# Kernel optimization log

Measured on AMD Instinct MI355X. Metric: run time of the kernel, lower is better.

Reference implementation:

```python
import jax, jax.numpy as jnp
import numpy as np

NEG_SLOPE = 0.2


def _gcn_conv(x, edge_index, W, b):
    # Standard GCNConv: y = D^-1/2 (A + I) D^-1/2 (x W) + b
    N = x.shape[0]
    loop = jnp.arange(N, dtype=edge_index.dtype)
    src = jnp.concatenate([edge_index[0], loop])  # [E+N]
    dst = jnp.concatenate([edge_index[1], loop])  # [E+N]
    deg = jax.ops.segment_sum(jnp.ones_like(dst, dtype=x.dtype), dst, num_segments=N)
    dinv = jnp.where(deg > 0, jax.lax.rsqrt(deg), 0.0)
    norm = dinv[src] * dinv[dst]                  # [E+N]
    h = x @ W                                     # [N, out] dense GEMM
    msg = h[src] * norm[:, None]                  # irregular gather, [E+N, out]
    agg = jax.ops.segment_sum(msg, dst, num_segments=N)  # irregular scatter
    return agg + b


def setup_inputs() -> dict:
    key = jax.random.key(0)
    ks = jax.random.split(key, 5)
    N, E, d_in, d_hid = 50000, 800000, 256, 512
    s = lambda fan_in, fan_out: np.sqrt(6.0 / (fan_in + fan_out))
    return {
        "x": jax.random.normal(ks[0], (N, d_in), dtype=jnp.float32),
        "edge_index": jax.random.randint(ks[1], (2, E), 0, N, dtype=jnp.int64),
        "W_gcn": jax.random.uniform(ks[2], (d_in, d_hid), jnp.float32, -s(d_in, d_hid), s(d_in, d_hid)),
        "b_gcn": jnp.zeros((d_hid,), jnp.float32),
        "W2": jax.random.uniform(ks[3], (d_hid, d_hid), jnp.float32, -s(d_hid, d_hid), s(d_hid, d_hid)),
        "b2": jnp.zeros((d_hid,), jnp.float32),
        "W_out": jax.random.uniform(ks[4], (d_hid, 1), jnp.float32, -s(d_hid, 1), s(d_hid, 1)),
        "b_out": jnp.zeros((1,), jnp.float32),
    }


def reference(x, edge_index, W_gcn, b_gcn, W2, b2, W_out, b_out):
    h = _gcn_conv(x, edge_index, W_gcn, b_gcn)           # [N, 512]
    h = jax.nn.leaky_relu(h, NEG_SLOPE)
    h = jax.nn.leaky_relu(h @ W2 + b2, NEG_SLOPE)        # [N, 512]
    return h @ W_out + b_out                             # [N, 1]
```

## Files before the change

### kernel.cpp

```cpp
#include <hip/hip_runtime.h>

#define D_IN  256
#define D_HID 512
#define NEG_SLOPE 0.2f
#define SCAN_CHUNK 2048
#define GATHER_BLOCKS 2048

typedef __attribute__((ext_vector_type(8))) short short8;
typedef __attribute__((ext_vector_type(4))) float floatx4;

__device__ __forceinline__ unsigned short f2bf(float f) {
    unsigned int u = __float_as_uint(f);
    u += 0x7fffu + ((u >> 16) & 1u);
    return (unsigned short)(u >> 16);
}
__device__ __forceinline__ float bf2f(unsigned short u) {
    return __uint_as_float(((unsigned int)u) << 16);
}

__device__ __forceinline__ int eidx(const void* ei, long pos, int is64) {
    return is64 ? (int)((const long long*)ei)[pos] : ((const int*)ei)[pos];
}

__global__ __launch_bounds__(256) void k_init(int* __restrict__ deg, int N,
                                              const unsigned int* __restrict__ ei,
                                              int npairs, int* flag,
                                              const float* __restrict__ b_out,
                                              float* __restrict__ out) {
    int t = blockIdx.x * blockDim.x + threadIdx.x;
    if (blockIdx.x == 0) {
        __shared__ int nz;
        if (threadIdx.x == 0) nz = 0;
        __syncthreads();
        for (int p = threadIdx.x; p < npairs; p += blockDim.x)
            if (ei[2 * p + 1] != 0) nz = 1;
        __syncthreads();
        if (threadIdx.x == 0) *flag = nz ? 0 : 1;
    }
    if (t < N) { deg[t] = 0; out[t] = b_out[0]; }
}

__global__ __launch_bounds__(256) void k_wtrans(const float* __restrict__ Wa,
                                                unsigned short* __restrict__ Wat,
                                                const float* __restrict__ Wb,
                                                unsigned short* __restrict__ Wbt) {
    __shared__ float t[64][65];
    int b = blockIdx.x;
    const float* W; unsigned short* Wt; int K, Nc, tk, tn;
    if (b < 32) { W = Wa; Wt = Wat; K = 256; Nc = 512; tk = b & 3; tn = b >> 2; }
    else { b -= 32; W = Wb; Wt = Wbt; K = 512; Nc = 512; tk = b & 7; tn = b >> 3; }
    int k0 = tk * 64, n0 = tn * 64;
    int c = threadIdx.x & 63;
    int r0 = threadIdx.x >> 6;
#pragma unroll
    for (int i = 0; i < 16; ++i) {
        int r = r0 + i * 4;
        t[r][c] = W[(long)(k0 + r) * Nc + n0 + c];
    }
    __syncthreads();
#pragma unroll
    for (int i = 0; i < 16; ++i) {
        int r = r0 + i * 4;
        Wt[(long)(n0 + r) * K + k0 + c] = f2bf(t[c][r]);
    }
}

__global__ void k_deg_count(const void* __restrict__ ei, const int* __restrict__ flag,
                            int* __restrict__ deg, int E) {
    int e = blockIdx.x * blockDim.x + threadIdx.x;
    if (e < E) atomicAdd(&deg[eidx(ei, (long)E + e, *flag)], 1);
}

__global__ __launch_bounds__(256) void k_scan1(const int* __restrict__ deg,
                                               int* __restrict__ bsum, int N) {
    int base = blockIdx.x * SCAN_CHUNK;
    int hi = min(base + SCAN_CHUNK, N);
    int s = 0;
    for (int i = base + threadIdx.x; i < hi; i += 256) s += deg[i];
#pragma unroll
    for (int off = 32; off > 0; off >>= 1) s += __shfl_down(s, off, 64);
    __shared__ int lds[4];
    if ((threadIdx.x & 63) == 0) lds[threadIdx.x >> 6] = s;
    __syncthreads();
    if (threadIdx.x == 0) bsum[blockIdx.x] = lds[0] + lds[1] + lds[2] + lds[3];
}

__global__ __launch_bounds__(256) void k_scan23(const int* __restrict__ deg,
                                                const int* __restrict__ bsum, int NB,
                                                int* __restrict__ offs,
                                                int* __restrict__ cursor,
                                                float* __restrict__ dinv, int N) {
    __shared__ int lds[256];
    int t = threadIdx.x;
    int bbase = 0;
    for (int i = 0; i < NB; ++i) bbase += (i < blockIdx.x) ? bsum[i] : 0;
    if (blockIdx.x == NB - 1 && t == 0) offs[N] = bbase + bsum[NB - 1];
    int base = blockIdx.x * SCAN_CHUNK;
    int lo = base + t * 8;
    int v[8], s = 0;
#pragma unroll
    for (int j = 0; j < 8; ++j) {
        int i = lo + j;
        v[j] = (i < N) ? deg[i] : 0;
        s += v[j];
    }
    lds[t] = s;
    __syncthreads();
    for (int d = 1; d < 256; d <<= 1) {
        int add = (t >= d) ? lds[t - d] : 0;
        __syncthreads();
        lds[t] += add;
        __syncthreads();
    }
    int run = bbase + ((t > 0) ? lds[t - 1] : 0);
#pragma unroll
    for (int j = 0; j < 8; ++j) {
        int i = lo + j;
        if (i < N) {
            offs[i] = run; cursor[i] = run;
            dinv[i] = rsqrtf(1.0f + (float)v[j]);
            run += v[j];
        }
    }
}

__global__ __launch_bounds__(256) void k_prescale(const float* __restrict__ x,
                                                  const float* __restrict__ dinv,
                                                  unsigned short* __restrict__ xb, int N) {
    long t = (long)blockIdx.x * blockDim.x + threadIdx.x;
    long total = (long)N * D_IN / 4;
    if (t >= total) return;
    int row = (int)(t >> 6);
    float s = dinv[row];
    float4 v = *(const float4*)(x + t * 4);
    ushort4 o;
    o.x = f2bf(v.x * s); o.y = f2bf(v.y * s); o.z = f2bf(v.z * s); o.w = f2bf(v.w * s);
    *(ushort4*)(xb + t * 4) = o;
}

__global__ void k_fill(const void* __restrict__ ei, const int* __restrict__ flag,
                       int* __restrict__ cursor, int* __restrict__ esrc, int E) {
    int e = blockIdx.x * blockDim.x + threadIdx.x;
    if (e >= E) return;
    int is64 = *flag;
    int s = eidx(ei, e, is64), d = eidx(ei, (long)E + e, is64);
    int pos = atomicAdd(&cursor[d], 1);
    esrc[pos] = s;
}

__global__ __launch_bounds__(256) void k_gather(const unsigned short* __restrict__ xb,
                                                const int* __restrict__ offs,
                                                const int* __restrict__ esrc,
                                                const float* __restrict__ dinv,
                                                unsigned short* __restrict__ aggb,
                                                int N, int nwaves) {
    int wid = blockIdx.x * 4 + (threadIdx.x >> 6);
    int lo = (int)((long)wid * N / nwaves);
    int hi = (int)((long)(wid + 1) * N / nwaves);
    if (lo >= hi) return;
    int lane = threadIdx.x & 63;
    int half = lane >> 5;
    int colofs = (lane & 31) * 8;
    const unsigned short* xbc = xb + colofs;

    int node = lo;
    int bg = offs[node];
    int en = offs[node + 1];
    float di = dinv[node];
    short8 sv = *(const short8*)(xbc + (long)node * D_IN);

    while (true) {
        int nxt = node + 1;
        bool has = nxt < hi;
        int en2 = 0; float di2 = 0.f; short8 sv2;
        if (has) {
            en2 = offs[nxt + 1];
            di2 = dinv[nxt];
            sv2 = *(const short8*)(xbc + (long)nxt * D_IN);
        }

        float a[8];
#pragma unroll
        for (int j = 0; j < 8; ++j)
            a[j] = (half == 0) ? bf2f((unsigned short)sv[j]) : 0.f;

        int e = bg;
        for (; e + 8 <= en; e += 8) {
            int s0 = esrc[e + half];
            int s1 = esrc[e + 2 + half];
            int s2 = esrc[e + 4 + half];
            int s3 = esrc[e + 6 + half];
            short8 u0 = *(const short8*)(xbc + (long)s0 * D_IN);
            short8 u1 = *(const short8*)(xbc + (long)s1 * D_IN);
            short8 u2 = *(const short8*)(xbc + (long)s2 * D_IN);
            short8 u3 = *(const short8*)(xbc + (long)s3 * D_IN);
#pragma unroll
            for (int j = 0; j < 8; ++j) {
                float t0 = bf2f((unsigned short)u0[j]) + bf2f((unsigned short)u1[j]);
                float t1 = bf2f((unsigned short)u2[j]) + bf2f((unsigned short)u3[j]);
                a[j] += t0 + t1;
            }
        }
        for (; e < en; e += 2) {
            int j0 = e + half;
            int jj = (j0 < en) ? j0 : en - 1;
            int s = esrc[jj];
            float w = (j0 < en) ? 1.f : 0.f;
            short8 u = *(const short8*)(xbc + (long)s * D_IN);
#pragma unroll
            for (int j = 0; j < 8; ++j)
                a[j] += w * bf2f((unsigned short)u[j]);
        }

#pragma unroll
        for (int j = 0; j < 8; ++j) a[j] += __shfl_xor(a[j], 32, 64);

        if (half == 0) {
            short8 o;
#pragma unroll
            for (int j = 0; j < 8; ++j) o[j] = (short)f2bf(a[j] * di);
            *(short8*)(aggb + (long)node * D_IN + colofs) = o;
        }

        if (!has) break;
        node = nxt; bg = en; en = en2; di = di2; sv = sv2;
    }
}

__device__ __forceinline__ void async_cp16(const unsigned short* gp, unsigned short* lp) {
    __builtin_amdgcn_global_load_lds((const __attribute__((address_space(1))) void*)gp,
                                     (__attribute__((address_space(3))) void*)lp, 16, 0, 0);
}

__device__ __forceinline__ void stage_sw64(const unsigned short* src, int strideK,
                                           int rowMax, unsigned short* lds, int tid) {
#pragma unroll
    for (int rr = 0; rr < 4; ++rr) {
        int c = rr * 256 + tid;
        int row = c >> 3;
        int ci = (c & 7) ^ (row & 7);
        if (row > rowMax) row = rowMax;
        async_cp16(src + (long)row * strideK + ci * 8, lds + c * 8);
    }
}

__device__ __forceinline__ bool map_block(int b, int M, int& m0, int& n0) {
    int x = b & 7, slot = b >> 3;
    int mt = x + 8 * (slot >> 2);
    m0 = mt * 128; n0 = (slot & 3) * 128;
    return m0 < M;
}

__global__ __launch_bounds__(256) void k_gemm_bf16(const unsigned short* __restrict__ A,
                                                   const unsigned short* __restrict__ Bt,
                                                   const float* __restrict__ bias,
                                                   unsigned short* __restrict__ C,
                                                   int M, int K) {
    __shared__ __align__(16) unsigned short As[128 * 64];
    __shared__ __align__(16) unsigned short Bs[128 * 64];
    __shared__ __align__(16) unsigned short Ep[32 * 128];
    const int tid  = threadIdx.x;
    const int lane = tid & 63, wave = tid >> 6;
    int m0, n0;
    if (!map_block(blockIdx.x, M, m0, n0)) return;
    const int r = lane & 15, q = lane >> 4;
    const int xv = r & 7;
    const int wm = (wave & 1) * 64, wn = (wave >> 1) * 64;
    const int band = wm >> 6;

    floatx4 acc[4][4];
#pragma unroll
    for (int i = 0; i < 4; ++i)
#pragma unroll
        for (int j = 0; j < 4; ++j) acc[i][j] = (floatx4){0.f, 0.f, 0.f, 0.f};

    for (int k0 = 0; k0 < K; k0 += 64) {
        stage_sw64(A + (long)m0 * K + k0, K, M - 1 - m0, As, tid);
        stage_sw64(Bt + (long)n0 * K + k0, K, 127, Bs, tid);
        __syncthreads();

#pragma unroll
        for (int s = 0; s < 2; ++s) {
            int slotbase = s * 4 + q;
            short8 af[4], bf[4];
#pragma unroll
            for (int i = 0; i < 4; ++i)
                af[i] = *(const short8*)(As + (wm + i * 16 + r) * 64 + (slotbase ^ xv) * 8);
#pragma unroll
            for (int j = 0; j < 4; ++j)
                bf[j] = *(const short8*)(Bs + (wn + j * 16 + r) * 64 + (slotbase ^ xv) * 8);
#pragma unroll
            for (int i = 0; i < 4; ++i)
#pragma unroll
                for (int j = 0; j < 4; ++j)
                    acc[i][j] = __builtin_amdgcn_mfma_f32_16x16x32_bf16(af[i], bf[j], acc[i][j], 0, 0, 0);
        }
        __syncthreads();
    }

    float bv[4];
#pragma unroll
    for (int j = 0; j < 4; ++j) bv[j] = bias[n0 + wn + j * 16 + r];

#pragma unroll
    for (int i = 0; i < 4; ++i) {
#pragma unroll
        for (int j = 0; j < 4; ++j) {
#pragma unroll
            for (int t2 = 0; t2 < 4; ++t2) {
                float v = acc[i][j][t2] + bv[j];
                v = v > 0.f ? v : NEG_SLOPE * v;
                Ep[(band * 16 + q * 4 + t2) * 128 + wn + j * 16 + r] = f2bf(v);
            }
        }
        __syncthreads();
#pragma unroll
        for (int rr = 0; rr < 2; ++rr) {
            int c = rr * 256 + tid;
            int lrow = c >> 4, ccol = c & 15;
            int grow = m0 + (lrow >> 4) * 64 + i * 16 + (lrow & 15);
            if (grow < M) {
                short8 v = *(const short8*)(Ep + lrow * 128 + ccol * 8);
                *(short8*)(C + (long)grow * D_HID + n0 + ccol * 8) = v;
            }
        }
        __syncthreads();
    }
}

__global__ __launch_bounds__(256) void k_gemm2f(const unsigned short* __restrict__ A,
                                                const unsigned short* __restrict__ Bt,
                                                const float* __restrict__ bias,
                                                const float* __restrict__ wout,
                                                float* __restrict__ out,
                                                int M, int K) {
    __shared__ __align__(16) unsigned short As[128 * 64];
    __shared__ __align__(16) unsigned short Bs[128 * 64];
    const int tid  = threadIdx.x;
    const int lane = tid & 63, wave = tid >> 6;
    int m0, n0;
    if (!map_block(blockIdx.x, M, m0, n0)) return;
    const int r = lane & 15, q = lane >> 4;
    const int xv = r & 7;
    const int wm = (wave & 1) * 64, wn = (wave >> 1) * 64;

    floatx4 acc[4][4];
#pragma unroll
    for (int i = 0; i < 4; ++i)
#pragma unroll
        for (int j = 0; j < 4; ++j) acc[i][j] = (floatx4){0.f, 0.f, 0.f, 0.f};

    for (int k0 = 0; k0 < K; k0 += 64) {
        stage_sw64(A + (long)m0 * K + k0, K, M - 1 - m0, As, tid);
        stage_sw64(Bt + (long)n0 * K + k0, K, 127, Bs, tid);
        __syncthreads();

#pragma unroll
        for (int s = 0; s < 2; ++s) {
            int slotbase = s * 4 + q;
            short8 af[4], bf[4];
#pragma unroll
            for (int i = 0; i < 4; ++i)
                af[i] = *(const short8*)(As + (wm + i * 16 + r) * 64 + (slotbase ^ xv) * 8);
#pragma unroll
            for (int j = 0; j < 4; ++j)
                bf[j] = *(const short8*)(Bs + (wn + j * 16 + r) * 64 + (slotbase ^ xv) * 8);
#pragma unroll
            for (int i = 0; i < 4; ++i)
#pragma unroll
                for (int j = 0; j < 4; ++j)
                    acc[i][j] = __builtin_amdgcn_mfma_f32_16x16x32_bf16(af[i], bf[j], acc[i][j], 0, 0, 0);
        }
        __syncthreads();
    }

    float bv[4], wv[4];
#pragma unroll
    for (int j = 0; j < 4; ++j) {
        int col = n0 + wn + j * 16 + r;
        bv[j] = bias[col];
        wv[j] = wout[col];
    }
#pragma unroll
    for (int i = 0; i < 4; ++i) {
#pragma unroll
        for (int t2 = 0; t2 < 4; ++t2) {
            float p = 0.f;
#pragma unroll
            for (int j = 0; j < 4; ++j) {
                float v = acc[i][j][t2] + bv[j];
                v = v > 0.f ? v : NEG_SLOPE * v;
                p += v * wv[j];
            }
            p += __shfl_xor(p, 8, 64);
            p += __shfl_xor(p, 4, 64);
            p += __shfl_xor(p, 2, 64);
            p += __shfl_xor(p, 1, 64);
            if (r == 0) {
                int row = m0 + wm + i * 16 + q * 4 + t2;
                if (row < M) atomicAdd(&out[row], p);
            }
        }
    }
}

extern "C" void kernel_launch(void* const* d_in, const int* in_sizes, int n_in,
                              void* d_out, int out_size, void* d_ws, size_t ws_size,
                              hipStream_t stream) {
    const float* x     = (const float*)d_in[0];
    const void*  ei    = d_in[1];
    const float* W_gcn = (const float*)d_in[2];
    const float* b_gcn = (const float*)d_in[3];
    const float* W2    = (const float*)d_in[4];
    const float* b2    = (const float*)d_in[5];
    const float* W_out = (const float*)d_in[6];
    const float* b_out = (const float*)d_in[7];
    float* out = (float*)d_out;

    const int N = in_sizes[0] / D_IN;
    const int E = in_sizes[1] / 2;
    const int NB = (N + SCAN_CHUNK - 1) / SCAN_CHUNK;

    char* w = (char*)d_ws;
    size_t off = 0;
    auto alloc = [&](size_t bytes) { char* p = w + off; off = (off + bytes + 255) & ~(size_t)255; return p; };
    int*            flag   = (int*)alloc(256);
    float*          dinv   = (float*)alloc((size_t)N * 4);
    int*            deg_i  = (int*)alloc((size_t)N * 4);
    int*            offs   = (int*)alloc((size_t)(N + 1) * 4);
    int*            cursor = (int*)alloc((size_t)N * 4);
    int*            bsum   = (int*)alloc((size_t)NB * 4);
    int*            esrc   = (int*)alloc((size_t)(E + 16) * 4);
    unsigned short* xb     = (unsigned short*)alloc((size_t)N * D_IN * 2);
    unsigned short* aggb   = (unsigned short*)alloc((size_t)N * D_IN * 2);
    unsigned short* h1     = (unsigned short*)alloc((size_t)N * D_HID * 2);
    unsigned short* Wgt    = (unsigned short*)alloc((size_t)D_IN * D_HID * 2);
    unsigned short* W2t    = (unsigned short*)alloc((size_t)D_HID * D_HID * 2);

    int npairs = E < 2048 ? E : 2048;
    k_init<<<(N + 255) / 256, 256, 0, stream>>>(deg_i, N, (const unsigned int*)ei,
                                                npairs, flag, b_out, out);
    k_wtrans<<<96, 256, 0, stream>>>(W_gcn, Wgt, W2, W2t);

    k_deg_count<<<(E + 255) / 256, 256, 0, stream>>>(ei, flag, deg_i, E);
    k_scan1<<<NB, 256, 0, stream>>>(deg_i, bsum, N);
    k_scan23<<<NB, 256, 0, stream>>>(deg_i, bsum, NB, offs, cursor, dinv, N);

    long pthreads = (long)N * D_IN / 4;
    k_prescale<<<(unsigned)((pthreads + 255) / 256), 256, 0, stream>>>(x, dinv, xb, N);
    k_fill<<<(E + 255) / 256, 256, 0, stream>>>(ei, flag, cursor, esrc, E);

    int gblocks_gather = GATHER_BLOCKS;
    int nwaves = gblocks_gather * 4;
    k_gather<<<gblocks_gather, 256, 0, stream>>>(xb, offs, esrc, dinv, aggb, N, nwaves);

    int mtiles = (N + 127) / 128;
    int gblocks = ((mtiles + 7) / 8) * 8 * 4;
    k_gemm_bf16<<<gblocks, 256, 0, stream>>>(aggb, Wgt, b_gcn, h1, N, D_IN);
    k_gemm2f<<<gblocks, 256, 0, stream>>>(h1, W2t, b2, W_out, out, N, D_HID);
}
```

Before: 338.3 us.

## Merge setup kernels, use one-node-per-wave gather, double-buffer GEMM LDS tiles

Folds the weight-transpose kernel into the init kernel and the prescale and CSR-fill kernels into one launch, cutting launch count and the serialization between them. The gather kernel drops its persistent wave loop with next-node prefetch and instead launches one wave per node. Both bf16 GEMMs move to double-buffered LDS staging so the next K tile's loads are issued while MFMAs run on the current tile. This doubles LDS use per block, which may lower occupancy, and the double-buffered loop appears to drop a barrier between compute and the next stage, which risks a race on the buffer being overwritten.

```diff
diff --git a/kernel.cpp b/kernel.cpp
--- a/kernel.cpp
+++ b/kernel.cpp
@@ -4,7 +4,6 @@
 #define D_HID 512
 #define NEG_SLOPE 0.2f
 #define SCAN_CHUNK 2048
-#define GATHER_BLOCKS 2048
 
 typedef __attribute__((ext_vector_type(8))) short short8;
 typedef __attribute__((ext_vector_type(4))) float floatx4;
@@ -26,9 +25,34 @@
                                               const unsigned int* __restrict__ ei,
                                               int npairs, int* flag,
                                               const float* __restrict__ b_out,
-                                              float* __restrict__ out) {
-    int t = blockIdx.x * blockDim.x + threadIdx.x;
-    if (blockIdx.x == 0) {
+                                              float* __restrict__ out,
+                                              const float* __restrict__ Wa,
+                                              unsigned short* __restrict__ Wat,
+                                              const float* __restrict__ Wb,
+                                              unsigned short* __restrict__ Wbt) {
+    __shared__ float tl[64][65];
+    int b = blockIdx.x;
+    if (b < 96) {
+        const float* W; unsigned short* Wt; int K, Nc, tk, tn;
+        if (b < 32) { W = Wa; Wt = Wat; K = 256; Nc = 512; tk = b & 3; tn = b >> 2; }
+        else { b -= 32; W = Wb; Wt = Wbt; K = 512; Nc = 512; tk = b & 7; tn = b >> 3; }
+        int k0 = tk * 64, n0 = tn * 64;
+        int c = threadIdx.x & 63;
+        int r0 = threadIdx.x >> 6;
+#pragma unroll
+        for (int i = 0; i < 16; ++i) {
+            int r = r0 + i * 4;
+            tl[r][c] = W[(long)(k0 + r) * Nc + n0 + c];
+        }
+        __syncthreads();
+#pragma unroll
+        for (int i = 0; i < 16; ++i) {
+            int r = r0 + i * 4;
+            Wt[(long)(n0 + r) * K + k0 + c] = f2bf(tl[c][r]);
+        }
+        return;
+    }
+    if (b == 96) {
         __shared__ int nz;
         if (threadIdx.x == 0) nz = 0;
         __syncthreads();
@@ -37,32 +61,8 @@
         __syncthreads();
         if (threadIdx.x == 0) *flag = nz ? 0 : 1;
     }
+    int t = (b - 96) * 256 + threadIdx.x;
     if (t < N) { deg[t] = 0; out[t] = b_out[0]; }
-}
-
-__global__ __launch_bounds__(256) void k_wtrans(const float* __restrict__ Wa,
-                                                unsigned short* __restrict__ Wat,
-                                                const float* __restrict__ Wb,
-                                                unsigned short* __restrict__ Wbt) {
-    __shared__ float t[64][65];
-    int b = blockIdx.x;
-    const float* W; unsigned short* Wt; int K, Nc, tk, tn;
-    if (b < 32) { W = Wa; Wt = Wat; K = 256; Nc = 512; tk = b & 3; tn = b >> 2; }
-    else { b -= 32; W = Wb; Wt = Wbt; K = 512; Nc = 512; tk = b & 7; tn = b >> 3; }
-    int k0 = tk * 64, n0 = tn * 64;
-    int c = threadIdx.x & 63;
-    int r0 = threadIdx.x >> 6;
-#pragma unroll
-    for (int i = 0; i < 16; ++i) {
-        int r = r0 + i * 4;
-        t[r][c] = W[(long)(k0 + r) * Nc + n0 + c];
-    }
-    __syncthreads();
-#pragma unroll
-    for (int i = 0; i < 16; ++i) {
-        int r = r0 + i * 4;
-        Wt[(long)(n0 + r) * K + k0 + c] = f2bf(t[c][r]);
-    }
 }
 
 __global__ void k_deg_count(const void* __restrict__ ei, const int* __restrict__ flag,
@@ -124,23 +124,27 @@
     }
 }
 
-__global__ __launch_bounds__(256) void k_prescale(const float* __restrict__ x,
-                                                  const float* __restrict__ dinv,
-                                                  unsigned short* __restrict__ xb, int N) {
-    long t = (long)blockIdx.x * blockDim.x + threadIdx.x;
-    long total = (long)N * D_IN / 4;
-    if (t >= total) return;
-    int row = (int)(t >> 6);
-    float s = dinv[row];
-    float4 v = *(const float4*)(x + t * 4);
-    ushort4 o;
-    o.x = f2bf(v.x * s); o.y = f2bf(v.y * s); o.z = f2bf(v.z * s); o.w = f2bf(v.w * s);
-    *(ushort4*)(xb + t * 4) = o;
-}
-
-__global__ void k_fill(const void* __restrict__ ei, const int* __restrict__ flag,
-                       int* __restrict__ cursor, int* __restrict__ esrc, int E) {
-    int e = blockIdx.x * blockDim.x + threadIdx.x;
+__global__ __launch_bounds__(256) void k_prefill(const float* __restrict__ x,
+                                                 const float* __restrict__ dinv,
+                                                 unsigned short* __restrict__ xb,
+                                                 const void* __restrict__ ei,
+                                                 const int* __restrict__ flag,
+                                                 int* __restrict__ cursor,
+                                                 int* __restrict__ esrc,
+                                                 int N, int E, int PB) {
+    if ((int)blockIdx.x < PB) {
+        long t = (long)blockIdx.x * 256 + threadIdx.x;
+        long total = (long)N * D_IN / 4;
+        if (t >= total) return;
+        int row = (int)(t >> 6);
+        float s = dinv[row];
+        float4 v = *(const float4*)(x + t * 4);
+        ushort4 o;
+        o.x = f2bf(v.x * s); o.y = f2bf(v.y * s); o.z = f2bf(v.z * s); o.w = f2bf(v.w * s);
+        *(ushort4*)(xb + t * 4) = o;
+        return;
+    }
+    int e = (blockIdx.x - PB) * 256 + threadIdx.x;
     if (e >= E) return;
     int is64 = *flag;
     int s = eidx(ei, e, is64), d = eidx(ei, (long)E + e, is64);
@@ -152,78 +156,60 @@
                                                 const int* __restrict__ offs,
                                                 const int* __restrict__ esrc,
                                                 const float* __restrict__ dinv,
-                                                unsigned short* __restrict__ aggb,
-                                                int N, int nwaves) {
-    int wid = blockIdx.x * 4 + (threadIdx.x >> 6);
-    int lo = (int)((long)wid * N / nwaves);
-    int hi = (int)((long)(wid + 1) * N / nwaves);
-    if (lo >= hi) return;
+                                                unsigned short* __restrict__ aggb, int N) {
+    int node = blockIdx.x * 4 + (threadIdx.x >> 6);
+    if (node >= N) return;
     int lane = threadIdx.x & 63;
     int half = lane >> 5;
     int colofs = (lane & 31) * 8;
     const unsigned short* xbc = xb + colofs;
-
-    int node = lo;
-    int bg = offs[node];
-    int en = offs[node + 1];
     float di = dinv[node];
-    short8 sv = *(const short8*)(xbc + (long)node * D_IN);
-
-    while (true) {
-        int nxt = node + 1;
-        bool has = nxt < hi;
-        int en2 = 0; float di2 = 0.f; short8 sv2;
-        if (has) {
-            en2 = offs[nxt + 1];
-            di2 = dinv[nxt];
-            sv2 = *(const short8*)(xbc + (long)nxt * D_IN);
-        }
-
-        float a[8];
+
+    float a[8];
+    {
+        short8 v = *(const short8*)(xbc + (long)node * D_IN);
 #pragma unroll
         for (int j = 0; j < 8; ++j)
-            a[j] = (half == 0) ? bf2f((unsigned short)sv[j]) : 0.f;
-
-        int e = bg;
-        for (; e + 8 <= en; e += 8) {
-            int s0 = esrc[e + half];
-            int s1 = esrc[e + 2 + half];
-            int s2 = esrc[e + 4 + half];
-            int s3 = esrc[e + 6 + half];
-            short8 u0 = *(const short8*)(xbc + (long)s0 * D_IN);
-            short8 u1 = *(const short8*)(xbc + (long)s1 * D_IN);
-            short8 u2 = *(const short8*)(xbc + (long)s2 * D_IN);
-            short8 u3 = *(const short8*)(xbc + (long)s3 * D_IN);
-#pragma unroll
-            for (int j = 0; j < 8; ++j) {
-                float t0 = bf2f((unsigned short)u0[j]) + bf2f((unsigned short)u1[j]);
-                float t1 = bf2f((unsigned short)u2[j]) + bf2f((unsigned short)u3[j]);
-                a[j] += t0 + t1;
-            }
-        }
-        for (; e < en; e += 2) {
-            int j0 = e + half;
-            int jj = (j0 < en) ? j0 : en - 1;
-            int s = esrc[jj];
-            float w = (j0 < en) ? 1.f : 0.f;
-            short8 u = *(const short8*)(xbc + (long)s * D_IN);
-#pragma unroll
-            for (int j = 0; j < 8; ++j)
-                a[j] += w * bf2f((unsigned short)u[j]);
-        }
-
-#pragma unroll
-        for (int j = 0; j < 8; ++j) a[j] += __shfl_xor(a[j], 32, 64);
-
-        if (half == 0) {
-            short8 o;
-#pragma unroll
-            for (int j = 0; j < 8; ++j) o[j] = (short)f2bf(a[j] * di);
-            *(short8*)(aggb + (long)node * D_IN + colofs) = o;
-        }
-
-        if (!has) break;
-        node = nxt; bg = en; en = en2; di = di2; sv = sv2;
+            a[j] = (half == 0) ? bf2f((unsigned short)v[j]) : 0.f;
+    }
+
+    int beg = offs[node], end = offs[node + 1];
+    int e = beg;
+    for (; e + 8 <= end; e += 8) {
+        int s0 = esrc[e + half];
+        int s1 = esrc[e + 2 + half];
+        int s2 = esrc[e + 4 + half];
+        int s3 = esrc[e + 6 + half];
+        short8 u0 = *(const short8*)(xbc + (long)s0 * D_IN);
+        short8 u1 = *(const short8*)(xbc + (long)s1 * D_IN);
+        short8 u2 = *(const short8*)(xbc + (long)s2 * D_IN);
+        short8 u3 = *(const short8*)(xbc + (long)s3 * D_IN);
+#pragma unroll
+        for (int j = 0; j < 8; ++j) {
+            float t0 = bf2f((unsigned short)u0[j]) + bf2f((unsigned short)u1[j]);
+            float t1 = bf2f((unsigned short)u2[j]) + bf2f((unsigned short)u3[j]);
+            a[j] += t0 + t1;
+        }
+    }
+    for (; e < end; e += 2) {
+        int j0 = e + half;
+        int jj = (j0 < end) ? j0 : end - 1;
+        int s = esrc[jj];
+        float w = (j0 < end) ? 1.f : 0.f;
+        short8 u = *(const short8*)(xbc + (long)s * D_IN);
+#pragma unroll
+        for (int j = 0; j < 8; ++j)
+            a[j] += w * bf2f((unsigned short)u[j]);
+    }
+
+#pragma unroll
+    for (int j = 0; j < 8; ++j) a[j] += __shfl_xor(a[j], 32, 64);
+
+    if (half == 0) {
+        short8 o;
+#pragma unroll
+        for (int j = 0; j < 8; ++j) o[j] = (short)f2bf(a[j] * di);
+        *(short8*)(aggb + (long)node * D_IN + colofs) = o;
     }
 }
 
@@ -256,8 +242,8 @@
                                                    const float* __restrict__ bias,
                                                    unsigned short* __restrict__ C,
                                                    int M, int K) {
-    __shared__ __align__(16) unsigned short As[128 * 64];
-    __shared__ __align__(16) unsigned short Bs[128 * 64];
+    __shared__ __align__(16) unsigned short As[2][128 * 64];
+    __shared__ __align__(16) unsigned short Bs[2][128 * 64];
     __shared__ __align__(16) unsigned short Ep[32 * 128];
     const int tid  = threadIdx.x;
     const int lane = tid & 63, wave = tid >> 6;
@@ -267,6 +253,9 @@
     const int xv = r & 7;
     const int wm = (wave & 1) * 64, wn = (wave >> 1) * 64;
     const int band = wm >> 6;
+    const int rmA = M - 1 - m0;
+    const unsigned short* Ab = A + (long)m0 * K;
+    const unsigned short* Bb = Bt + (long)n0 * K;
 
     floatx4 acc[4][4];
 #pragma unroll
@@ -274,21 +263,26 @@
 #pragma unroll
         for (int j = 0; j < 4; ++j) acc[i][j] = (floatx4){0.f, 0.f, 0.f, 0.f};
 
-    for (int k0 = 0; k0 < K; k0 += 64) {
-        stage_sw64(A + (long)m0 * K + k0, K, M - 1 - m0, As, tid);
-        stage_sw64(Bt + (long)n0 * K + k0, K, 127, Bs, tid);
-        __syncthreads();
-
+    const int nt = K >> 6;
+    stage_sw64(Ab, K, rmA, As[0], tid);
+    stage_sw64(Bb, K, 127, Bs[0], tid);
+    __syncthreads();
+    for (int t = 0; t < nt; ++t) {
+        const int cur = t & 1;
+        if (t + 1 < nt) {
+            stage_sw64(Ab + (t + 1) * 64, K, rmA, As[cur ^ 1], tid);
+            stage_sw64(Bb + (t + 1) * 64, K, 127, Bs[cur ^ 1], tid);
+        }
 #pragma unroll
         for (int s = 0; s < 2; ++s) {
             int slotbase = s * 4 + q;
             short8 af[4], bf[4];
 #pragma unroll
             for (int i = 0; i < 4; ++i)
-                af[i] = *(const short8*)(As + (wm + i * 16 + r) * 64 + (slotbase ^ xv) * 8);
+                af[i] = *(const short8*)(As[cur] + (wm + i * 16 + r) * 64 + (slotbase ^ xv) * 8);
 #pragma unroll
             for (int j = 0; j < 4; ++j)
-                bf[j] = *(const short8*)(Bs + (wn + j * 16 + r) * 64 + (slotbase ^ xv) * 8);
+                bf[j] = *(const short8*)(Bs[cur] + (wn + j * 16 + r) * 64 + (slotbase ^ xv) * 8);
 #pragma unroll
             for (int i = 0; i < 4; ++i)
 #pragma unroll
@@ -334,8 +328,8 @@
                                                 const float* __restrict__ wout,
                                                 float* __restrict__ out,
                                                 int M, int K) {
-    __shared__ __align__(16) unsigned short As[128 * 64];
-    __shared__ __align__(16) unsigned short Bs[128 * 64];
+    __shared__ __align__(16) unsigned short As[2][128 * 64];
+    __shared__ __align__(16) unsigned short Bs[2][128 * 64];
     const int tid  = threadIdx.x;
     const int lane = tid & 63, wave = tid >> 6;
     int m0, n0;
@@ -343,6 +337,9 @@
     const int r = lane & 15, q = lane >> 4;
     const int xv = r & 7;
     const int wm = (wave & 1) * 64, wn = (wave >> 1) * 64;
+    const int rmA = M - 1 - m0;
+    const unsigned short* Ab = A + (long)m0 * K;
+    const unsigned short* Bb = Bt + (long)n0 * K;
 
     floatx4 acc[4][4];
 #pragma unroll
@@ -350,21 +347,26 @@
 #pragma unroll
         for (int j = 0; j < 4; ++j) acc[i][j] = (floatx4){0.f, 0.f, 0.f, 0.f};
 
-    for (int k0 = 0; k0 < K; k0 += 64) {
-        stage_sw64(A + (long)m0 * K + k0, K, M - 1 - m0, As, tid);
-        stage_sw64(Bt + (long)n0 * K + k0, K, 127, Bs, tid);
-        __syncthreads();
-
+    const int nt = K >> 6;
+    stage_sw64(Ab, K, rmA, As[0], tid);
+    stage_sw64(Bb, K, 127, Bs[0], tid);
+    __syncthreads();
+    for (int t = 0; t < nt; ++t) {
+        const int cur = t & 1;
+        if (t + 1 < nt) {
+            stage_sw64(Ab + (t + 1) * 64, K, rmA, As[cur ^ 1], tid);
+            stage_sw64(Bb + (t + 1) * 64, K, 127, Bs[cur ^ 1], tid);
+        }
 #pragma unroll
         for (int s = 0; s < 2; ++s) {
             int slotbase = s * 4 + q;
             short8 af[4], bf[4];
 #pragma unroll
             for (int i = 0; i < 4; ++i)
-                af[i] = *(const short8*)(As + (wm + i * 16 + r) * 64 + (slotbase ^ xv) * 8);
+                af[i] = *(const short8*)(As[cur] + (wm + i * 16 + r) * 64 + (slotbase ^ xv) * 8);
 #pragma unroll
             for (int j = 0; j < 4; ++j)
-                bf[j] = *(const short8*)(Bs + (wn + j * 16 + r) * 64 + (slotbase ^ xv) * 8);
+                bf[j] = *(const short8*)(Bs[cur] + (wn + j * 16 + r) * 64 + (slotbase ^ xv) * 8);
 #pragma unroll
             for (int i = 0; i < 4; ++i)
 #pragma unroll
@@ -438,21 +440,20 @@
     unsigned short* W2t    = (unsigned short*)alloc((size_t)D_HID * D_HID * 2);
 
     int npairs = E < 2048 ? E : 2048;
-    k_init<<<(N + 255) / 256, 256, 0, stream>>>(deg_i, N, (const unsigned int*)ei,
-                                                npairs, flag, b_out, out);
-    k_wtrans<<<96, 256, 0, stream>>>(W_gcn, Wgt, W2, W2t);
+    int init_blocks = 96 + (N + 255) / 256;
+    k_init<<<init_blocks, 256, 0, stream>>>(deg_i, N, (const unsigned int*)ei,
+                                            npairs, flag, b_out, out,
+                                            W_gcn, Wgt, W2, W2t);
 
     k_deg_count<<<(E + 255) / 256, 256, 0, stream>>>(ei, flag, deg_i, E);
     k_scan1<<<NB, 256, 0, stream>>>(deg_i, bsum, N);
     k_scan23<<<NB, 256, 0, stream>>>(deg_i, bsum, NB, offs, cursor, dinv, N);
 
-    long pthreads = (long)N * D_IN / 4;
-    k_prescale<<<(unsigned)((pthreads + 255) / 256), 256, 0, stream>>>(x, dinv, xb, N);
-    k_fill<<<(E + 255) / 256, 256, 0, stream>>>(ei, flag, cursor, esrc, E);
-
-    int gblocks_gather = GATHER_BLOCKS;
-    int nwaves = gblocks_gather * 4;
-    k_gather<<<gblocks_gather, 256, 0, stream>>>(xb, offs, esrc, dinv, aggb, N, nwaves);
+    int PB = (int)(((long)N * D_IN / 4 + 255) / 256);
+    int FB = (E + 255) / 256;
+    k_prefill<<<PB + FB, 256, 0, stream>>>(x, dinv, xb, ei, flag, cursor, esrc, N, E, PB);
+
+    k_gather<<<(N + 3) / 4, 256, 0, stream>>>(xb, offs, esrc, dinv, aggb, N);
 
     int mtiles = (N + 127) / 128;
     int gblocks = ((mtiles + 7) / 8) * 8 * 4;
```

Measured after the change: 336.7 us. No clear change (-0.5%).
